# Optimization experiments

Measured on AMD Instinct MI355X. Metric: run time of the kernel, lower is better.

Reference implementation:

```python
import jax, jax.numpy as jnp
import numpy as np

NUM_LAYERS = 3

def setup_inputs() -> dict:
    key = jax.random.key(0)
    ku, ki, ke1, ke2 = jax.random.split(key, 4)
    num_users, num_items, D, E = 100000, 50000, 128, 1000000
    # xavier-uniform-ish init scale for the embedding tables
    bound = float(np.sqrt(6.0 / (num_users + D)))
    user_w = jax.random.uniform(ku, (num_users, D), jnp.float32, -bound, bound)
    bound_i = float(np.sqrt(6.0 / (num_items + D)))
    item_w = jax.random.uniform(ki, (num_items, D), jnp.float32, -bound_i, bound_i)
    # bipartite edges: user -> item (item ids offset by num_users), plus reverse direction
    u = jax.random.randint(ke1, (E,), 0, num_users, dtype=jnp.int32)
    v = jax.random.randint(ke2, (E,), 0, num_items, dtype=jnp.int32) + num_users
    edge_index = jnp.stack([jnp.concatenate([u, v]), jnp.concatenate([v, u])])  # [2, 2E]
    return {"user_w": user_w, "item_w": item_w, "edge_index": edge_index,
            "num_users": num_users, "num_items": num_items}

def reference(user_w, item_w, edge_index, num_users, num_items):
    n_nodes = num_users + num_items
    src, dst = edge_index[0], edge_index[1]
    # degree via scatter-add (duplicate edges sum, same as coalesce)
    deg = jax.ops.segment_sum(jnp.ones_like(src, dtype=user_w.dtype), src,
                              num_segments=n_nodes)
    dinv = jnp.where(deg > 0, deg ** -0.5, 0.0)
    dinv = jnp.where(jnp.isfinite(dinv), dinv, 0.0)
    vals = dinv[src] * dinv[dst]  # normalized adjacency values, [2E]

    emb = jnp.concatenate([user_w, item_w], axis=0)  # [n_nodes, D]
    acc = emb
    x = emb
    for _ in range(NUM_LAYERS):
        # SpMM: out[s] += vals(e) * x[dst(e)]
        x = jax.ops.segment_sum(vals[:, None] * x[dst], src, num_segments=n_nodes)
        acc = acc + x
    final = acc / jnp.asarray(NUM_LAYERS + 1, dtype=emb.dtype)
    return final[:num_users], final[num_users:]
```

## Files before the change

### kernel.cpp

```cpp
#include <hip/hip_runtime.h>
#include <hip/hip_fp16.h>
#include <cstdint>
#include <cstddef>

#define D 128
#define BSH 9
#define BNODES 512
#define NBMAX 512
#define CCHUNK 8192


__global__ __launch_bounds__(256)
void k_hist_tohalf(const int* __restrict__ src, int* __restrict__ bhist,
                   int ne2, int nb, int nbh,
                   const float2* __restrict__ uw, const float2* __restrict__ iw,
                   __half2* __restrict__ x0, int nu2, int ntot2) {
    if ((int)blockIdx.x < nbh) {
        __shared__ int lc[NBMAX];
        for (int i = threadIdx.x; i < nb; i += 256) lc[i] = 0;
        __syncthreads();
        int base = blockIdx.x * CCHUNK;
        int lim = min(base + CCHUNK, ne2);
        for (int e = base + threadIdx.x; e < lim; e += 256)
            atomicAdd(&lc[src[e] >> BSH], 1);
        __syncthreads();
        for (int i = threadIdx.x; i < nb; i += 256)
            if (lc[i]) atomicAdd(&bhist[i], lc[i]);
    } else {
        int g = (blockIdx.x - nbh) * 256 + threadIdx.x;
        if (g < ntot2) {
            float2 v = (g < nu2) ? uw[g] : iw[g - nu2];
            x0[g] = __floats2half2_rn(v.x, v.y);
        }
    }
}

__global__ void k_bscan(const int* __restrict__ bhist, int* __restrict__ bbase,
                        int* __restrict__ bfill, int* __restrict__ rp,
                        int nb, int nn, int ne2) {
    __shared__ int a[NBMAX], b2[NBMAX];
    int t = threadIdx.x;
    int v = (t < nb) ? bhist[t] : 0;
    a[t] = v;
    __syncthreads();
    int* cur = a; int* nxt = b2;
    for (int o = 1; o < NBMAX; o <<= 1) {
        int x = cur[t];
        if (t >= o) x += cur[t - o];
        nxt[t] = x;
        __syncthreads();
        int* tm = cur; cur = nxt; nxt = tm;
    }
    int excl = cur[t] - v;
    if (t < nb) { bbase[t] = excl; bfill[t] = excl; }
    if (t == 0) { bbase[nb] = ne2; rp[nn] = ne2; }
}

__global__ __launch_bounds__(256)
void k_scatter(const int* __restrict__ src, const int* __restrict__ dst,
               int* __restrict__ bfill, int2* __restrict__ tmp, int ne2, int nb) {
    __shared__ int lc[NBMAX], lb[NBMAX];
    for (int i = threadIdx.x; i < nb; i += 256) lc[i] = 0;
    __syncthreads();
    int base = blockIdx.x * CCHUNK;
    int rec[CCHUNK / 256];
#pragma unroll
    for (int i = 0; i < CCHUNK / 256; ++i) {
        int e = base + i * 256 + threadIdx.x;
        rec[i] = -1;
        if (e < ne2) {
            int b = src[e] >> BSH;
            int r = atomicAdd(&lc[b], 1);
            rec[i] = (r << BSH) | b;
        }
    }
    __syncthreads();
    for (int i = threadIdx.x; i < nb; i += 256)
        if (lc[i]) lb[i] = atomicAdd(&bfill[i], lc[i]);
    __syncthreads();
#pragma unroll
    for (int i = 0; i < CCHUNK / 256; ++i) {
        if (rec[i] >= 0) {
            int e = base + i * 256 + threadIdx.x;
            int b = rec[i] & (BNODES - 1);
            int r = rec[i] >> BSH;
            tmp[lb[b] + r] = make_int2(src[e], dst[e]);
        }
    }
}

__global__ __launch_bounds__(256)
void k_build(const int2* __restrict__ tmp, const int* __restrict__ bbase,
             int* __restrict__ col, int* __restrict__ rp, float* __restrict__ dinv,
             float* __restrict__ dinv2, float* __restrict__ rinv, int nn) {
    __shared__ int cnt[BNODES];
    __shared__ int off[BNODES];
    __shared__ int wtot[4], woff[4];
    int bkt = blockIdx.x;
    int n0 = bkt << BSH;
    int nloc = min(BNODES, nn - n0);
    int ebeg = bbase[bkt], eend = bbase[bkt + 1];
    for (int i = threadIdx.x; i < BNODES; i += 256) cnt[i] = 0;
    __syncthreads();
    for (int e = ebeg + threadIdx.x; e < eend; e += 256)
        atomicAdd(&cnt[tmp[e].x - n0], 1);
    __syncthreads();
    int t = threadIdx.x;
    int c0 = cnt[2 * t], c1 = cnt[2 * t + 1];
    int s = c0 + c1;
    int lane = t & 63, wid = t >> 6;
    int x = s;
#pragma unroll
    for (int o = 1; o < 64; o <<= 1) {
        int y = __shfl_up(x, o);
        if (lane >= o) x += y;
    }
    if (lane == 63) wtot[wid] = x;
    __syncthreads();
    if (t == 0) { int a = 0; for (int k = 0; k < 4; ++k) { woff[k] = a; a += wtot[k]; } }
    __syncthreads();
    int eb = woff[wid] + x - s;
    off[2 * t] = eb;
    off[2 * t + 1] = eb + c0;
    __syncthreads();
    for (int i = threadIdx.x; i < nloc; i += 256) {
        rp[n0 + i] = ebeg + off[i];
        int c = cnt[i];
        float fc = (float)c;
        dinv[n0 + i]  = (c > 0) ? rsqrtf(fc) : 0.0f;
        dinv2[n0 + i] = (c > 0) ? 1.0f / fc : 0.0f;
        rinv[n0 + i]  = (c > 0) ? sqrtf(fc) : 0.0f;
    }
    __syncthreads();
    for (int i = threadIdx.x; i < BNODES; i += 256) cnt[i] = 0;
    __syncthreads();
    for (int e = ebeg + threadIdx.x; e < eend; e += 256) {
        int2 ed = tmp[e];
        int sl = ed.x - n0;
        int r = atomicAdd(&cnt[sl], 1);
        col[ebeg + off[sl] + r] = ed.y;
    }
}

template <int MODE>
__global__ __launch_bounds__(256)
void k_spmm(const float4* __restrict__ xin, float4* __restrict__ xout,
            const int* __restrict__ rp, const int* __restrict__ col,
            const float* __restrict__ dinv, const float* __restrict__ dinv2,
            const float* __restrict__ rinv,
            const float4* __restrict__ x0h, const float4* __restrict__ y1h,
            float4* __restrict__ outp, int nn) {
    int wave = (blockIdx.x * blockDim.x + threadIdx.x) >> 6;
    int lane = threadIdx.x & 63;
    int g = lane >> 4, l16 = lane & 15;
    int node = wave * 4 + g;
    int beg = 0, end = 0;
    if (node < nn) { beg = rp[node]; end = rp[node + 1]; }
    float acc[8];
#pragma unroll
    for (int k = 0; k < 8; ++k) acc[k] = 0.f;

    int srcl = g << 4;
    for (int base = beg; base < end; base += 16) {
        int p = base + l16;
        int d = 0;
        float wt = 0.f;
        if (p < end) {
            d = col[p];
            if (MODE == 0) wt = dinv[d];
        }
        int m = min(16, end - base);
#pragma unroll 8
        for (int t = 0; t < m; ++t) {
            int dd = __shfl(d, srcl + t);
            float4 rv = xin[(size_t)dd * 16 + l16];
            const __half2* hp = reinterpret_cast<const __half2*>(&rv);
            if (MODE == 0) {
                float wv = __shfl(wt, srcl + t);
#pragma unroll
                for (int k = 0; k < 4; ++k) {
                    float2 f = __half22float2(hp[k]);
                    acc[2 * k]     = fmaf(wv, f.x, acc[2 * k]);
                    acc[2 * k + 1] = fmaf(wv, f.y, acc[2 * k + 1]);
                }
            } else {
#pragma unroll
                for (int k = 0; k < 4; ++k) {
                    float2 f = __half22float2(hp[k]);
                    acc[2 * k]     += f.x;
                    acc[2 * k + 1] += f.y;
                }
            }
        }
    }
    if (node >= nn) return;
    float s2 = dinv2[node];
    if (MODE != 2) {
        __half2 h[4];
#pragma unroll
        for (int k = 0; k < 4; ++k)
            h[k] = __floats2half2_rn(s2 * acc[2 * k], s2 * acc[2 * k + 1]);
        xout[(size_t)node * 16 + l16] = *reinterpret_cast<const float4*>(h);
    } else {
        size_t r16 = (size_t)node * 16 + l16;
        float4 ev = x0h[r16];
        float4 av = y1h[r16];
        float4 bv = xin[r16];
        const __half2* ep = reinterpret_cast<const __half2*>(&ev);
        const __half2* ap = reinterpret_cast<const __half2*>(&av);
        const __half2* bp = reinterpret_cast<const __half2*>(&bv);
        float rv = rinv[node];
        float o[8];
#pragma unroll
        for (int k = 0; k < 4; ++k) {
            float2 fe = __half22float2(ep[k]);
            float2 fa = __half22float2(ap[k]);
            float2 fb = __half22float2(bp[k]);
            o[2 * k]     = 0.25f * (fe.x + (fa.x + fb.x + s2 * acc[2 * k]) * rv);
            o[2 * k + 1] = 0.25f * (fe.y + (fa.y + fb.y + s2 * acc[2 * k + 1]) * rv);
        }
        float4 w0 = make_float4(o[0], o[1], o[2], o[3]);
        float4 w1 = make_float4(o[4], o[5], o[6], o[7]);
        size_t r32 = (size_t)node * 32 + 2 * l16;
        outp[r32] = w0;
        outp[r32 + 1] = w1;
    }
}


extern "C" void kernel_launch(void* const* d_in, const int* in_sizes, int n_in,
                              void* d_out, int out_size, void* d_ws, size_t ws_size,
                              hipStream_t stream) {
    const float* uw = (const float*)d_in[0];
    const float* iw = (const float*)d_in[1];
    const int* ei = (const int*)d_in[2];

    const int NU = in_sizes[0] / D;
    const int NI = in_sizes[1] / D;
    const int NN = NU + NI;
    const int NE2 = in_sizes[2] / 2;
    const int* src = ei;
    const int* dst = ei + NE2;
    const int NB = (NN + BNODES - 1) >> BSH;

    char* p = (char*)d_ws;
    auto alloc = [&](size_t bytes) -> void* {
        void* r = (void*)p;
        p += (bytes + 255) & ~(size_t)255;
        return r;
    };
    int* bhist  = (int*)alloc(NBMAX * 4);
    int* bbase  = (int*)alloc((NBMAX + 1) * 4);
    int* bfill  = (int*)alloc(NBMAX * 4);
    int* rp     = (int*)alloc((size_t)(NN + 1) * 4);
    float* dinv = (float*)alloc((size_t)NN * 4);
    float* dinv2= (float*)alloc((size_t)NN * 4);
    float* rinv = (float*)alloc((size_t)NN * 4);
    int2* tmp   = (int2*)alloc((size_t)NE2 * 8);
    int* col    = (int*)alloc((size_t)NE2 * 4);
    __half2* xa = (__half2*)alloc((size_t)NN * D * 2);
    __half2* xb = (__half2*)alloc((size_t)NN * D * 2);
    __half2* xc = (__half2*)alloc((size_t)NN * D * 2);
    float* outp = (float*)d_out;

    hipMemsetAsync(bhist, 0, NBMAX * 4, stream);

    int ntot2 = NN * (D / 2);
    int nu2 = NU * (D / 2);
    int bce = (NE2 + CCHUNK - 1) / CCHUNK;
    int bi = (ntot2 + 255) / 256;

    k_hist_tohalf<<<bce + bi, 256, 0, stream>>>(src, bhist, NE2, NB, bce,
                                                (const float2*)uw, (const float2*)iw,
                                                xa, nu2, ntot2);
    k_bscan<<<1, NBMAX, 0, stream>>>(bhist, bbase, bfill, rp, NB, NN, NE2);
    k_scatter<<<bce, 256, 0, stream>>>(src, dst, bfill, tmp, NE2, NB);
    k_build<<<NB, 256, 0, stream>>>(tmp, bbase, col, rp, dinv, dinv2, rinv, NN);

    int bs = (NN + 15) / 16;
    k_spmm<0><<<bs, 256, 0, stream>>>((const float4*)xa, (float4*)xb, rp, col,
                                      dinv, dinv2, rinv, nullptr, nullptr, nullptr, NN);
    k_spmm<1><<<bs, 256, 0, stream>>>((const float4*)xb, (float4*)xc, rp, col,
                                      dinv, dinv2, rinv, nullptr, nullptr, nullptr, NN);
    k_spmm<2><<<bs, 256, 0, stream>>>((const float4*)xc, nullptr, rp, col,
                                      dinv, dinv2, rinv,
                                      (const float4*)xa, (const float4*)xb,
                                      (float4*)outp, NN);
}
```

Baseline: 442.5 us.

## Store scaled SpMM features in FP8 and pack edge temp records into 32 bits

Result: faster. 391.9 us (-11.5%).

```diff
diff --git a/kernel.cpp b/kernel.cpp
--- a/kernel.cpp
+++ b/kernel.cpp
@@ -8,6 +8,21 @@
 #define BNODES 512
 #define NBMAX 512
 #define CCHUNK 8192
+#define FP8_SCALE 2048.0f
+#define FP8_INV_SCALE (1.0f / 2048.0f)
+
+typedef float v2f __attribute__((ext_vector_type(2)));
+
+static __device__ inline unsigned pack_fp8x4(float a, float b, float c, float d) {
+    a = fminf(fmaxf(a, -440.f), 440.f);
+    b = fminf(fmaxf(b, -440.f), 440.f);
+    c = fminf(fmaxf(c, -440.f), 440.f);
+    d = fminf(fmaxf(d, -440.f), 440.f);
+    int r = 0;
+    r = __builtin_amdgcn_cvt_pk_fp8_f32(a, b, r, false);
+    r = __builtin_amdgcn_cvt_pk_fp8_f32(c, d, r, true);
+    return (unsigned)r;
+}
 
 
 __global__ __launch_bounds__(256)
@@ -58,7 +73,7 @@
 
 __global__ __launch_bounds__(256)
 void k_scatter(const int* __restrict__ src, const int* __restrict__ dst,
-               int* __restrict__ bfill, int2* __restrict__ tmp, int ne2, int nb) {
+               int* __restrict__ bfill, int* __restrict__ tmp, int ne2, int nb) {
     __shared__ int lc[NBMAX], lb[NBMAX];
     for (int i = threadIdx.x; i < nb; i += 256) lc[i] = 0;
     __syncthreads();
@@ -84,15 +99,16 @@
             int e = base + i * 256 + threadIdx.x;
             int b = rec[i] & (BNODES - 1);
             int r = rec[i] >> BSH;
-            tmp[lb[b] + r] = make_int2(src[e], dst[e]);
+            tmp[lb[b] + r] = ((src[e] & (BNODES - 1)) << 18) | dst[e];
         }
     }
 }
 
 __global__ __launch_bounds__(256)
-void k_build(const int2* __restrict__ tmp, const int* __restrict__ bbase,
-             int* __restrict__ col, int* __restrict__ rp, float* __restrict__ dinv,
-             float* __restrict__ dinv2, float* __restrict__ rinv, int nn) {
+void k_build(const int* __restrict__ tmp, const int* __restrict__ bbase,
+             int* __restrict__ col, int* __restrict__ rp,
+             float* __restrict__ dinv2, float* __restrict__ rinv,
+             const float4* __restrict__ x0h, uint2* __restrict__ y0p, int nn) {
     __shared__ int cnt[BNODES];
     __shared__ int off[BNODES];
     __shared__ int wtot[4], woff[4];
@@ -103,7 +119,7 @@
     for (int i = threadIdx.x; i < BNODES; i += 256) cnt[i] = 0;
     __syncthreads();
     for (int e = ebeg + threadIdx.x; e < eend; e += 256)
-        atomicAdd(&cnt[tmp[e].x - n0], 1);
+        atomicAdd(&cnt[tmp[e] >> 18], 1);
     __syncthreads();
     int t = threadIdx.x;
     int c0 = cnt[2 * t], c1 = cnt[2 * t + 1];
@@ -127,28 +143,43 @@
         rp[n0 + i] = ebeg + off[i];
         int c = cnt[i];
         float fc = (float)c;
-        dinv[n0 + i]  = (c > 0) ? rsqrtf(fc) : 0.0f;
         dinv2[n0 + i] = (c > 0) ? 1.0f / fc : 0.0f;
         rinv[n0 + i]  = (c > 0) ? sqrtf(fc) : 0.0f;
     }
+    {
+        int r = threadIdx.x >> 4;
+        int l = threadIdx.x & 15;
+        for (; r < nloc; r += 16) {
+            int c = cnt[r];
+            float sc = (c > 0) ? FP8_SCALE * rsqrtf((float)c) : 0.0f;
+            float4 v = x0h[(size_t)(n0 + r) * 16 + l];
+            const __half2* hp = reinterpret_cast<const __half2*>(&v);
+            float2 f0 = __half22float2(hp[0]), f1 = __half22float2(hp[1]);
+            float2 f2 = __half22float2(hp[2]), f3 = __half22float2(hp[3]);
+            uint2 o;
+            o.x = pack_fp8x4(sc * f0.x, sc * f0.y, sc * f1.x, sc * f1.y);
+            o.y = pack_fp8x4(sc * f2.x, sc * f2.y, sc * f3.x, sc * f3.y);
+            y0p[(size_t)(n0 + r) * 16 + l] = o;
+        }
+    }
     __syncthreads();
     for (int i = threadIdx.x; i < BNODES; i += 256) cnt[i] = 0;
     __syncthreads();
     for (int e = ebeg + threadIdx.x; e < eend; e += 256) {
-        int2 ed = tmp[e];
-        int sl = ed.x - n0;
+        int v = tmp[e];
+        int sl = v >> 18;
         int r = atomicAdd(&cnt[sl], 1);
-        col[ebeg + off[sl] + r] = ed.y;
+        col[ebeg + off[sl] + r] = v & 0x3FFFF;
     }
 }
 
 template <int MODE>
 __global__ __launch_bounds__(256)
-void k_spmm(const float4* __restrict__ xin, float4* __restrict__ xout,
+void k_spmm(const uint2* __restrict__ yin, uint2* __restrict__ y8out,
+            float4* __restrict__ h16out, const float4* __restrict__ aux1,
+            const float4* __restrict__ aux2,
             const int* __restrict__ rp, const int* __restrict__ col,
-            const float* __restrict__ dinv, const float* __restrict__ dinv2,
-            const float* __restrict__ rinv,
-            const float4* __restrict__ x0h, const float4* __restrict__ y1h,
+            const float* __restrict__ dinv2, const float* __restrict__ rinv,
             float4* __restrict__ outp, int nn) {
     int wave = (blockIdx.x * blockDim.x + threadIdx.x) >> 6;
     int lane = threadIdx.x & 63;
@@ -156,68 +187,67 @@
     int node = wave * 4 + g;
     int beg = 0, end = 0;
     if (node < nn) { beg = rp[node]; end = rp[node + 1]; }
-    float acc[8];
-#pragma unroll
-    for (int k = 0; k < 8; ++k) acc[k] = 0.f;
+    v2f acc[4];
+#pragma unroll
+    for (int k = 0; k < 4; ++k) acc[k] = (v2f)(0.f);
 
     int srcl = g << 4;
     for (int base = beg; base < end; base += 16) {
         int p = base + l16;
-        int d = 0;
-        float wt = 0.f;
-        if (p < end) {
-            d = col[p];
-            if (MODE == 0) wt = dinv[d];
-        }
+        int d = (p < end) ? col[p] : 0;
         int m = min(16, end - base);
 #pragma unroll 8
         for (int t = 0; t < m; ++t) {
             int dd = __shfl(d, srcl + t);
-            float4 rv = xin[(size_t)dd * 16 + l16];
-            const __half2* hp = reinterpret_cast<const __half2*>(&rv);
-            if (MODE == 0) {
-                float wv = __shfl(wt, srcl + t);
-#pragma unroll
-                for (int k = 0; k < 4; ++k) {
-                    float2 f = __half22float2(hp[k]);
-                    acc[2 * k]     = fmaf(wv, f.x, acc[2 * k]);
-                    acc[2 * k + 1] = fmaf(wv, f.y, acc[2 * k + 1]);
-                }
-            } else {
-#pragma unroll
-                for (int k = 0; k < 4; ++k) {
-                    float2 f = __half22float2(hp[k]);
-                    acc[2 * k]     += f.x;
-                    acc[2 * k + 1] += f.y;
-                }
-            }
+            uint2 u = yin[(size_t)dd * 16 + l16];
+            acc[0] += __builtin_amdgcn_cvt_pk_f32_fp8((int)u.x, false);
+            acc[1] += __builtin_amdgcn_cvt_pk_f32_fp8((int)u.x, true);
+            acc[2] += __builtin_amdgcn_cvt_pk_f32_fp8((int)u.y, false);
+            acc[3] += __builtin_amdgcn_cvt_pk_f32_fp8((int)u.y, true);
         }
     }
     if (node >= nn) return;
     float s2 = dinv2[node];
+    size_t r16 = (size_t)node * 16 + l16;
     if (MODE != 2) {
+        float yv[8];
+#pragma unroll
+        for (int k = 0; k < 4; ++k) {
+            yv[2 * k]     = s2 * acc[k].x;
+            yv[2 * k + 1] = s2 * acc[k].y;
+        }
+        uint2 o8;
+        o8.x = pack_fp8x4(yv[0], yv[1], yv[2], yv[3]);
+        o8.y = pack_fp8x4(yv[4], yv[5], yv[6], yv[7]);
+        y8out[r16] = o8;
+        if (MODE == 1) {
+            float4 av = aux1[r16];
+            const __half2* ap = reinterpret_cast<const __half2*>(&av);
+#pragma unroll
+            for (int k = 0; k < 4; ++k) {
+                float2 fa = __half22float2(ap[k]);
+                yv[2 * k]     += fa.x;
+                yv[2 * k + 1] += fa.y;
+            }
+        }
         __half2 h[4];
 #pragma unroll
         for (int k = 0; k < 4; ++k)
-            h[k] = __floats2half2_rn(s2 * acc[2 * k], s2 * acc[2 * k + 1]);
-        xout[(size_t)node * 16 + l16] = *reinterpret_cast<const float4*>(h);
+            h[k] = __floats2half2_rn(yv[2 * k], yv[2 * k + 1]);
+        h16out[r16] = *reinterpret_cast<const float4*>(h);
     } else {
-        size_t r16 = (size_t)node * 16 + l16;
-        float4 ev = x0h[r16];
-        float4 av = y1h[r16];
-        float4 bv = xin[r16];
+        float4 ev = aux1[r16];
+        float4 zv = aux2[r16];
         const __half2* ep = reinterpret_cast<const __half2*>(&ev);
-        const __half2* ap = reinterpret_cast<const __half2*>(&av);
-        const __half2* bp = reinterpret_cast<const __half2*>(&bv);
-        float rv = rinv[node];
+        const __half2* zp = reinterpret_cast<const __half2*>(&zv);
+        float rs = rinv[node] * FP8_INV_SCALE;
         float o[8];
 #pragma unroll
         for (int k = 0; k < 4; ++k) {
             float2 fe = __half22float2(ep[k]);
-            float2 fa = __half22float2(ap[k]);
-            float2 fb = __half22float2(bp[k]);
-            o[2 * k]     = 0.25f * (fe.x + (fa.x + fb.x + s2 * acc[2 * k]) * rv);
-            o[2 * k + 1] = 0.25f * (fe.y + (fa.y + fb.y + s2 * acc[2 * k + 1]) * rv);
+            float2 fz = __half22float2(zp[k]);
+            o[2 * k]     = 0.25f * (fe.x + (fz.x + s2 * acc[k].x) * rs);
+            o[2 * k + 1] = 0.25f * (fe.y + (fz.y + s2 * acc[k].y) * rs);
         }
         float4 w0 = make_float4(o[0], o[1], o[2], o[3]);
         float4 w1 = make_float4(o[4], o[5], o[6], o[7]);
@@ -249,19 +279,21 @@
         p += (bytes + 255) & ~(size_t)255;
         return r;
     };
-    int* bhist  = (int*)alloc(NBMAX * 4);
-    int* bbase  = (int*)alloc((NBMAX + 1) * 4);
-    int* bfill  = (int*)alloc(NBMAX * 4);
-    int* rp     = (int*)alloc((size_t)(NN + 1) * 4);
-    float* dinv = (float*)alloc((size_t)NN * 4);
-    float* dinv2= (float*)alloc((size_t)NN * 4);
-    float* rinv = (float*)alloc((size_t)NN * 4);
-    int2* tmp   = (int2*)alloc((size_t)NE2 * 8);
-    int* col    = (int*)alloc((size_t)NE2 * 4);
-    __half2* xa = (__half2*)alloc((size_t)NN * D * 2);
-    __half2* xb = (__half2*)alloc((size_t)NN * D * 2);
-    __half2* xc = (__half2*)alloc((size_t)NN * D * 2);
-    float* outp = (float*)d_out;
+    int* bhist   = (int*)alloc(NBMAX * 4);
+    int* bbase   = (int*)alloc((NBMAX + 1) * 4);
+    int* bfill   = (int*)alloc(NBMAX * 4);
+    int* rp      = (int*)alloc((size_t)(NN + 1) * 4);
+    float* dinv2 = (float*)alloc((size_t)NN * 4);
+    float* rinv  = (float*)alloc((size_t)NN * 4);
+    int* col     = (int*)alloc((size_t)NE2 * 4);
+    __half2* zh  = (__half2*)alloc((size_t)NN * D * 2);
+    int* tmp     = (int*)zh;
+    __half2* xa  = (__half2*)alloc((size_t)NN * D * 2);
+    uint2* y0p   = (uint2*)alloc((size_t)NN * D);
+    uint2* y1p   = (uint2*)alloc((size_t)NN * D);
+    __half2* y1h = (__half2*)alloc((size_t)NN * D * 2);
+    uint2* y2p   = y0p;
+    float* outp  = (float*)d_out;
 
     hipMemsetAsync(bhist, 0, NBMAX * 4, stream);
 
@@ -275,15 +307,17 @@
                                                 xa, nu2, ntot2);
     k_bscan<<<1, NBMAX, 0, stream>>>(bhist, bbase, bfill, rp, NB, NN, NE2);
     k_scatter<<<bce, 256, 0, stream>>>(src, dst, bfill, tmp, NE2, NB);
-    k_build<<<NB, 256, 0, stream>>>(tmp, bbase, col, rp, dinv, dinv2, rinv, NN);
+    k_build<<<NB, 256, 0, stream>>>(tmp, bbase, col, rp, dinv2, rinv,
+                                    (const float4*)xa, y0p, NN);
 
     int bs = (NN + 15) / 16;
-    k_spmm<0><<<bs, 256, 0, stream>>>((const float4*)xa, (float4*)xb, rp, col,
-                                      dinv, dinv2, rinv, nullptr, nullptr, nullptr, NN);
-    k_spmm<1><<<bs, 256, 0, stream>>>((const float4*)xb, (float4*)xc, rp, col,
-                                      dinv, dinv2, rinv, nullptr, nullptr, nullptr, NN);
-    k_spmm<2><<<bs, 256, 0, stream>>>((const float4*)xc, nullptr, rp, col,
-                                      dinv, dinv2, rinv,
-                                      (const float4*)xa, (const float4*)xb,
-                                      (float4*)outp, NN);
-}
+    k_spmm<0><<<bs, 256, 0, stream>>>((const uint2*)y0p, y1p, (float4*)y1h,
+                                      nullptr, nullptr, rp, col, dinv2, rinv,
+                                      nullptr, NN);
+    k_spmm<1><<<bs, 256, 0, stream>>>((const uint2*)y1p, y2p, (float4*)zh,
+                                      (const float4*)y1h, nullptr, rp, col,
+                                      dinv2, rinv, nullptr, NN);
+    k_spmm<2><<<bs, 256, 0, stream>>>((const uint2*)y2p, nullptr, nullptr,
+                                      (const float4*)xa, (const float4*)zh,
+                                      rp, col, dinv2, rinv, (float4*)outp, NN);
+}
```
